# Optimization experiments

Hardware: AMD Instinct MI355X
Metric: run time of the kernel (lower is better)

## Reference

```python
import jax, jax.numpy as jnp
import numpy as np

HEADS = 8
DIM_HEAD = 64


def setup_inputs() -> dict:
    key = jax.random.key(0)
    ks = jax.random.split(key, 10)
    B, NQ, NK, D, INNER = 4, 2048, 2048, 1024, HEADS * DIM_HEAD
    w_scale = 0.02
    return {
        "x": jax.random.normal(ks[0], (B, NQ, D), jnp.float32),
        "context": jax.random.normal(ks[1], (B, NK, D), jnp.float32),
        "wq": jax.random.normal(ks[2], (D, INNER), jnp.float32) * w_scale,
        "bq": jax.random.normal(ks[3], (INNER,), jnp.float32) * w_scale,
        "wk": jax.random.normal(ks[4], (D, INNER), jnp.float32) * w_scale,
        "bk": jax.random.normal(ks[5], (INNER,), jnp.float32) * w_scale,
        "wv": jax.random.normal(ks[6], (D, INNER), jnp.float32) * w_scale,
        "bv": jax.random.normal(ks[7], (INNER,), jnp.float32) * w_scale,
        "wo": jax.random.normal(ks[8], (INNER, D), jnp.float32) * w_scale,
        "bo": jax.random.normal(ks[9], (D,), jnp.float32) * w_scale,
    }


def _split_heads(t):
    # [b, n, h*d] -> [b, h, n, d]
    b, n, _ = t.shape
    return t.reshape(b, n, HEADS, DIM_HEAD).transpose(0, 2, 1, 3)


def reference(x, context, wq, bq, wk, bk, wv, bv, wo, bo):
    scale = DIM_HEAD ** -0.5
    q = _split_heads(x @ wq + bq)        # [b, h, nq, d]
    k = _split_heads(context @ wk + bk)  # [b, h, nk, d]
    v = _split_heads(context @ wv + bv)  # [b, h, nk, d]
    sim = jnp.einsum('bhid,bhjd->bhij', q, k) * scale  # full score matrix, as in original
    attn = jax.nn.softmax(sim, axis=-1)
    out = jnp.einsum('bhij,bhjd->bhid', attn, v)       # [b, h, nq, d]
    b, h, n, d = out.shape
    out = out.transpose(0, 2, 1, 3).reshape(b, n, h * d)
    return out @ wo + bo
```

## Files before the change

kernel.cpp:

```cpp
#include <hip/hip_runtime.h>
#include <hip/hip_bf16.h>

typedef __attribute__((ext_vector_type(8))) short short8;
typedef __attribute__((ext_vector_type(4))) float f32x4;
typedef __attribute__((ext_vector_type(2))) unsigned uint2u;

__device__ __forceinline__ short f2bf(float f) {
  union { float f; unsigned u; } x; x.f = f;
  unsigned r = x.u + 0x7fffu + ((x.u >> 16) & 1u);
  return (short)(r >> 16);
}

__device__ __forceinline__ void gload16(const short* g, short* l) {
  __builtin_amdgcn_global_load_lds(
      (const __attribute__((address_space(1))) unsigned*)g,
      (__attribute__((address_space(3))) unsigned*)l, 16, 0, 0);
}

__global__ void cast2_bf16_kernel(const float* __restrict__ a,
                                  const float* __restrict__ b,
                                  short* __restrict__ dst) {
  int i = (blockIdx.x * 256 + threadIdx.x) * 4;
  const float* s = (i < (1 << 23)) ? a : b;
  int j = i & ((1 << 23) - 1);
  float4 f = *(const float4*)(s + j);
  union { short s[4]; uint2 u; } o;
  o.s[0] = f2bf(f.x); o.s[1] = f2bf(f.y);
  o.s[2] = f2bf(f.z); o.s[3] = f2bf(f.w);
  *(uint2*)(dst + i) = o.u;
}

__global__ __launch_bounds__(256) void transpose_cast4_kernel(
    const float* __restrict__ wq, const float* __restrict__ wk,
    const float* __restrict__ wv, const float* __restrict__ wo,
    short* __restrict__ wqt, short* __restrict__ wkt,
    short* __restrict__ wvt, short* __restrict__ wot) {
  __shared__ short tile[64][72];
  int z = blockIdx.z;
  const float* src = (z == 0) ? wq : (z == 1) ? wk : (z == 2) ? wv : wo;
  short* dst = (z == 0) ? wqt : (z == 1) ? wkt : (z == 2) ? wvt : wot;
  int R = (z < 3) ? 1024 : 512, C = (z < 3) ? 512 : 1024;
  int tpc = C >> 6;
  int bx = blockIdx.x % tpc, by = blockIdx.x / tpc;
  int r0 = by * 64, c0 = bx * 64;
  int tx = threadIdx.x & 15, ty = threadIdx.x >> 4;
#pragma unroll
  for (int i = 0; i < 4; i++) {
    int r = i * 16 + ty;
    float4 f = *(const float4*)(src + (size_t)(r0 + r) * C + c0 + tx * 4);
    union { short s[4]; uint2 u; } o;
    o.s[0] = f2bf(f.x); o.s[1] = f2bf(f.y);
    o.s[2] = f2bf(f.z); o.s[3] = f2bf(f.w);
    *(uint2*)&tile[r][tx * 4] = o.u;
  }
  __syncthreads();
#pragma unroll
  for (int i = 0; i < 4; i++) {
    int c = i * 16 + ty;
    union { short s[4]; uint2 u; } o;
#pragma unroll
    for (int k = 0; k < 4; k++) o.s[k] = tile[tx * 4 + k][c];
    *(uint2*)(dst + (size_t)(c0 + c) * R + r0 + tx * 4) = o.u;
  }
}

__device__ __forceinline__ void gemm_core(
    const short* __restrict__ A, const short* __restrict__ Bt, int K,
    int mblk, int nblk, short* sA, short* sB, f32x4 (&acc)[4][4]) {
  int tid = threadIdx.x;
  int lane = tid & 63, wave = tid >> 6;
  int quad = lane >> 4, l15 = lane & 15;
  int wm = (wave >> 1) * 64, wn = (wave & 1) * 64;
  int sub = lane >> 3, e8 = lane & 7;
  int swz = (e8 ^ sub) << 3;
  int s0 = (quad ^ (l15 & 7)) << 3;
  const short* Ag = A + (size_t)(mblk + 32 * wave + sub) * K + swz;
  const short* Bg = Bt + (size_t)(nblk + 32 * wave + sub) * K + swz;
  short* Al = sA + 4 * wave * 512;
  short* Bl = sB + 4 * wave * 512;

  for (int k0 = 0; k0 < K; k0 += 64) {
    __syncthreads();
#pragma unroll
    for (int t = 0; t < 4; t++) {
      gload16(Ag + (size_t)(8 * t) * K + k0, Al + t * 512);
      gload16(Bg + (size_t)(8 * t) * K + k0, Bl + t * 512);
    }
    __syncthreads();
#pragma unroll
    for (int h = 0; h < 2; h++) {
      int so = s0 ^ (h << 5);
      short8 af[4], bf[4];
#pragma unroll
      for (int mt = 0; mt < 4; mt++)
        af[mt] = *(const short8*)(&sA[(wm + mt * 16 + l15) * 64 + so]);
#pragma unroll
      for (int nt = 0; nt < 4; nt++)
        bf[nt] = *(const short8*)(&sB[(wn + nt * 16 + l15) * 64 + so]);
#pragma unroll
      for (int mt = 0; mt < 4; mt++)
#pragma unroll
        for (int nt = 0; nt < 4; nt++)
          acc[mt][nt] = __builtin_amdgcn_mfma_f32_16x16x32_bf16(
              af[mt], bf[nt], acc[mt][nt], 0, 0, 0);
    }
  }
}

__global__ __launch_bounds__(256) void gemm_qkv(
    const short* __restrict__ xb, const short* __restrict__ cb,
    const short* __restrict__ wqt, const short* __restrict__ wkt,
    const short* __restrict__ wvt,
    const float* __restrict__ bq, const float* __restrict__ bk,
    const float* __restrict__ bv,
    short* __restrict__ Qb, short* __restrict__ Kb, short* __restrict__ Vt) {
  __shared__ __align__(16) short sA[128 * 64];
  __shared__ __align__(16) short sB[128 * 64];
  int z = blockIdx.z;
  const short* A  = (z == 0) ? xb : cb;
  const short* Bt = (z == 0) ? wqt : (z == 1) ? wkt : wvt;
  const float* bias = (z == 0) ? bq : (z == 1) ? bk : bv;
  short* out = (z == 0) ? Qb : (z == 1) ? Kb : Vt;
  float scale = (z == 0) ? 0.18033688011112042f : 1.0f;
  int mblk = blockIdx.x * 128, nblk = blockIdx.y * 128;
  f32x4 acc[4][4] = {};
  gemm_core(A, Bt, 1024, mblk, nblk, sA, sB, acc);

  int lane = threadIdx.x & 63, wave = threadIdx.x >> 6;
  int quad = lane >> 4, l15 = lane & 15;
  int wm = (wave >> 1) * 64, wn = (wave & 1) * 64;
#pragma unroll
  for (int nt = 0; nt < 4; nt++) {
    int col = nblk + wn + nt * 16 + l15;
    float bias_v = bias[col];
    int h = col >> 6, dh = col & 63;
#pragma unroll
    for (int mt = 0; mt < 4; mt++)
#pragma unroll
      for (int r = 0; r < 4; r++) {
        int row = mblk + wm + mt * 16 + quad * 4 + r;
        float v = (acc[mt][nt][r] + bias_v) * scale;
        int b = row >> 11, n = row & 2047;
        size_t base = ((size_t)(b * 8 + h)) << 17;
        size_t idx = (z == 2) ? base + ((size_t)dh << 11) + n
                              : base + ((size_t)n << 6) + dh;
        out[idx] = f2bf(v);
      }
  }
}

__global__ __launch_bounds__(256) void gemm_out(
    const short* __restrict__ Ob, const short* __restrict__ wot,
    const float* __restrict__ bo, float* __restrict__ out) {
  __shared__ __align__(16) short sA[128 * 64];
  __shared__ __align__(16) short sB[128 * 64];
  int mblk = blockIdx.x * 128, nblk = blockIdx.y * 128;
  f32x4 acc[4][4] = {};
  gemm_core(Ob, wot, 512, mblk, nblk, sA, sB, acc);
  int lane = threadIdx.x & 63, wave = threadIdx.x >> 6;
  int quad = lane >> 4, l15 = lane & 15;
  int wm = (wave >> 1) * 64, wn = (wave & 1) * 64;
#pragma unroll
  for (int nt = 0; nt < 4; nt++) {
    int col = nblk + wn + nt * 16 + l15;
    float bias_v = bo[col];
#pragma unroll
    for (int mt = 0; mt < 4; mt++)
#pragma unroll
      for (int r = 0; r < 4; r++) {
        int row = mblk + wm + mt * 16 + quad * 4 + r;
        out[(size_t)row * 1024 + col] = acc[mt][nt][r] + bias_v;
      }
  }
}

__global__ __launch_bounds__(256, 2) void attn_kernel(
    const short* __restrict__ Qb, const short* __restrict__ Kb,
    const short* __restrict__ Vt, short* __restrict__ Ob) {
  __shared__ __align__(16) short sK[2 * 64 * 64];
  __shared__ __align__(16) short sV[2 * 64 * 64];
  int tid = threadIdx.x;
  int lane = tid & 63, wave = tid >> 6;
  int quad = lane >> 4, l15 = lane & 15;
  int bh = blockIdx.x & 31, qt = blockIdx.x >> 5;
  const short* Qp = Qb + ((size_t)bh << 17);
  const short* Kp = Kb + ((size_t)bh << 17);
  const short* Vp = Vt + ((size_t)bh << 17);
  int qrow0 = qt * 128 + wave * 32;

  short8 qf[2][2];
#pragma unroll
  for (int g = 0; g < 2; g++) {
    const short* qrow = Qp + (size_t)(qrow0 + g * 16 + l15) * 64;
    qf[g][0] = *(const short8*)(qrow + quad * 8);
    qf[g][1] = *(const short8*)(qrow + 32 + quad * 8);
  }

  int jk0 = 2 * wave, jk1 = 2 * wave + 1;
  int sub = lane >> 3;
  int e8  = lane & 7;
  int swz = (e8 ^ sub) << 3;
  const short* kg0 = Kp + (size_t)(8 * jk0 + sub) * 64 + e8 * 8;
  const short* kg1 = Kp + (size_t)(8 * jk1 + sub) * 64 + e8 * 8;
  const short* vg0 = Vp + (size_t)(8 * jk0 + sub) * 2048 + e8 * 8;
  const short* vg1 = Vp + (size_t)(8 * jk1 + sub) * 2048 + e8 * 8;
  int kw0 = (8 * jk0 + sub) * 64 + swz;
  int kw1 = (8 * jk1 + sub) * 64 + swz;

  int s0 = (quad ^ (l15 & 7)) << 3;
  int s1 = s0 ^ 32;

  f32x4 o[2][4] = {};
  float lsum[2] = {0.f, 0.f};

  uint4 rk0 = *(const uint4*)kg0, rk1 = *(const uint4*)kg1;
  uint4 rv0 = *(const uint4*)vg0, rv1 = *(const uint4*)vg1;
  *(uint4*)(sK + kw0) = rk0; *(uint4*)(sK + kw1) = rk1;
  *(uint4*)(sV + kw0) = rv0; *(uint4*)(sV + kw1) = rv1;
  rk0 = *(const uint4*)(kg0 + 4096); rk1 = *(const uint4*)(kg1 + 4096);
  rv0 = *(const uint4*)(vg0 + 64);   rv1 = *(const uint4*)(vg1 + 64);
  __syncthreads();

  for (int it = 0; it < 32; ++it) {
    const short* sKr = sK + (it & 1) * 4096;
    const short* sVr = sV + (it & 1) * 4096;
    if (it < 31) {
      short* sKw = sK + ((it & 1) ^ 1) * 4096;
      short* sVw = sV + ((it & 1) ^ 1) * 4096;
      *(uint4*)(sKw + kw0) = rk0; *(uint4*)(sKw + kw1) = rk1;
      *(uint4*)(sVw + kw0) = rv0; *(uint4*)(sVw + kw1) = rv1;
      if (it < 30) {
        size_t ko = (size_t)(it + 2) * 4096, vo = (size_t)(it + 2) * 64;
        rk0 = *(const uint4*)(kg0 + ko); rk1 = *(const uint4*)(kg1 + ko);
        rv0 = *(const uint4*)(vg0 + vo); rv1 = *(const uint4*)(vg1 + vo);
      }
    }
    unsigned xp[2][4][2];
#pragma unroll
    for (int jt = 0; jt < 4; jt++) {
      short8 k0 = *(const short8*)(&sKr[(jt * 16 + l15) * 64 + s0]);
      short8 k1 = *(const short8*)(&sKr[(jt * 16 + l15) * 64 + s1]);
#pragma unroll
      for (int g = 0; g < 2; g++) {
        f32x4 zz = {0.f, 0.f, 0.f, 0.f};
        zz = __builtin_amdgcn_mfma_f32_16x16x32_bf16(k0, qf[g][0], zz, 0, 0, 0);
        f32x4 st = __builtin_amdgcn_mfma_f32_16x16x32_bf16(k1, qf[g][1], zz, 0, 0, 0);
        float p0 = exp2f(st[0]), p1 = exp2f(st[1]);
        float p2 = exp2f(st[2]), p3 = exp2f(st[3]);
        lsum[g] += (p0 + p1) + (p2 + p3);
        union { __hip_bfloat162 b; unsigned u; } a0, a1;
        a0.b = __float22bfloat162_rn(make_float2(p0, p1));
        a1.b = __float22bfloat162_rn(make_float2(p2, p3));
        xp[g][jt][0] = a0.u; xp[g][jt][1] = a1.u;
      }
    }
    short8 pf[2][2];
#pragma unroll
    for (int g = 0; g < 2; g++) {
#pragma unroll
      for (int hb = 0; hb < 2; hb++) {
        unsigned x0 = xp[g][2 * hb][0], x1 = xp[g][2 * hb][1];
        unsigned x2 = xp[g][2 * hb + 1][0], x3 = xp[g][2 * hb + 1][1];
        uint2u r1 = __builtin_amdgcn_permlane32_swap(x0, x2, false, false);
        uint2u r2 = __builtin_amdgcn_permlane16_swap(r1[0], r1[1], false, false);
        uint2u r3 = __builtin_amdgcn_permlane32_swap(x1, x3, false, false);
        uint2u r4 = __builtin_amdgcn_permlane16_swap(r3[0], r3[1], false, false);
        union { unsigned u[4]; short8 s; } P;
        P.u[0] = r2[0]; P.u[1] = r4[0]; P.u[2] = r2[1]; P.u[3] = r4[1];
        pf[g][hb] = P.s;
      }
    }
#pragma unroll
    for (int nt = 0; nt < 4; nt++) {
      short8 v0 = *(const short8*)(&sVr[(nt * 16 + l15) * 64 + s0]);
      short8 v1 = *(const short8*)(&sVr[(nt * 16 + l15) * 64 + s1]);
#pragma unroll
      for (int g = 0; g < 2; g++) {
        o[g][nt] = __builtin_amdgcn_mfma_f32_16x16x32_bf16(v0, pf[g][0], o[g][nt], 0, 0, 0);
        o[g][nt] = __builtin_amdgcn_mfma_f32_16x16x32_bf16(v1, pf[g][1], o[g][nt], 0, 0, 0);
      }
    }
    if (it < 31) __syncthreads();
  }

  int b = bh >> 3, h = bh & 7;
#pragma unroll
  for (int g = 0; g < 2; g++) {
    float l = lsum[g];
    l += __shfl_xor(l, 16, 64);
    l += __shfl_xor(l, 32, 64);
    float inv = 1.0f / l;
    size_t rowbase = ((size_t)b * 2048 + qrow0 + g * 16 + l15) * 512 + h * 64 + quad * 4;
#pragma unroll
    for (int nt = 0; nt < 4; nt++) {
      union { short s[4]; uint2 u; } pk2;
#pragma unroll
      for (int r = 0; r < 4; r++) pk2.s[r] = f2bf(o[g][nt][r] * inv);
      *(uint2*)(Ob + rowbase + nt * 16) = pk2.u;
    }
  }
}

extern "C" void kernel_launch(void* const* d_in, const int* in_sizes, int n_in,
                              void* d_out, int out_size, void* d_ws, size_t ws_size,
                              hipStream_t stream) {
  const float* x   = (const float*)d_in[0];
  const float* ctx = (const float*)d_in[1];
  const float* wq  = (const float*)d_in[2];
  const float* bq  = (const float*)d_in[3];
  const float* wk  = (const float*)d_in[4];
  const float* bk  = (const float*)d_in[5];
  const float* wv  = (const float*)d_in[6];
  const float* bv  = (const float*)d_in[7];
  const float* wo  = (const float*)d_in[8];
  const float* bo  = (const float*)d_in[9];
  float* out = (float*)d_out;
  char* ws = (char*)d_ws;

  short* xb  = (short*)(ws);
  short* cb  = (short*)(ws + (16ull << 20));
  short* wqt = (short*)(ws + (32ull << 20));
  short* wkt = (short*)(ws + (33ull << 20));
  short* wvt = (short*)(ws + (34ull << 20));
  short* wot = (short*)(ws + (35ull << 20));
  short* Qb  = (short*)(ws + (36ull << 20));
  short* Kb  = (short*)(ws + (44ull << 20));
  short* Vt  = (short*)(ws + (52ull << 20));
  short* Ob  = (short*)(ws + (60ull << 20));

  cast2_bf16_kernel<<<16384, 256, 0, stream>>>(x, ctx, xb);
  transpose_cast4_kernel<<<dim3(128, 1, 4), 256, 0, stream>>>(
      wq, wk, wv, wo, wqt, wkt, wvt, wot);
  gemm_qkv<<<dim3(64, 4, 3), 256, 0, stream>>>(xb, cb, wqt, wkt, wvt,
                                               bq, bk, bv, Qb, Kb, Vt);
  attn_kernel<<<512, 256, 0, stream>>>(Qb, Kb, Vt, Ob);
  gemm_out<<<dim3(64, 8), 256, 0, stream>>>(Ob, wot, bo, out);
}
```

Baseline: 248.0 us.

## Vectorize GEMM epilogues via swapped MFMA operands, add setprio and hardware bf16 pack

```diff
diff --git a/kernel.cpp b/kernel.cpp
--- a/kernel.cpp
+++ b/kernel.cpp
@@ -11,10 +11,21 @@
   return (short)(r >> 16);
 }
 
+__device__ __forceinline__ unsigned cvt_pk_bf16(float a, float b) {
+  unsigned r;
+  asm("v_cvt_pk_bf16_f32 %0, %1, %2" : "=v"(r) : "v"(a), "v"(b));
+  return r;
+}
+
 __device__ __forceinline__ void gload16(const short* g, short* l) {
   __builtin_amdgcn_global_load_lds(
       (const __attribute__((address_space(1))) unsigned*)g,
       (__attribute__((address_space(3))) unsigned*)l, 16, 0, 0);
+}
+
+__device__ __forceinline__ void barrier_lgkm() {
+  asm volatile("s_waitcnt lgkmcnt(0)" ::: "memory");
+  __builtin_amdgcn_s_barrier();
 }
 
 __global__ void cast2_bf16_kernel(const float* __restrict__ a,
@@ -64,6 +75,7 @@
   }
 }
 
+template <bool SWAP>
 __device__ __forceinline__ void gemm_core(
     const short* __restrict__ A, const short* __restrict__ Bt, int K,
     int mblk, int nblk, short* sA, short* sB, f32x4 (&acc)[4][4]) {
@@ -100,9 +112,14 @@
 #pragma unroll
       for (int mt = 0; mt < 4; mt++)
 #pragma unroll
-        for (int nt = 0; nt < 4; nt++)
-          acc[mt][nt] = __builtin_amdgcn_mfma_f32_16x16x32_bf16(
-              af[mt], bf[nt], acc[mt][nt], 0, 0, 0);
+        for (int nt = 0; nt < 4; nt++) {
+          if (SWAP)
+            acc[mt][nt] = __builtin_amdgcn_mfma_f32_16x16x32_bf16(
+                bf[nt], af[mt], acc[mt][nt], 0, 0, 0);
+          else
+            acc[mt][nt] = __builtin_amdgcn_mfma_f32_16x16x32_bf16(
+                af[mt], bf[nt], acc[mt][nt], 0, 0, 0);
+        }
     }
   }
 }
@@ -123,29 +140,50 @@
   short* out = (z == 0) ? Qb : (z == 1) ? Kb : Vt;
   float scale = (z == 0) ? 0.18033688011112042f : 1.0f;
   int mblk = blockIdx.x * 128, nblk = blockIdx.y * 128;
-  f32x4 acc[4][4] = {};
-  gemm_core(A, Bt, 1024, mblk, nblk, sA, sB, acc);
-
   int lane = threadIdx.x & 63, wave = threadIdx.x >> 6;
   int quad = lane >> 4, l15 = lane & 15;
   int wm = (wave >> 1) * 64, wn = (wave & 1) * 64;
-#pragma unroll
-  for (int nt = 0; nt < 4; nt++) {
-    int col = nblk + wn + nt * 16 + l15;
-    float bias_v = bias[col];
-    int h = col >> 6, dh = col & 63;
-#pragma unroll
-    for (int mt = 0; mt < 4; mt++)
-#pragma unroll
-      for (int r = 0; r < 4; r++) {
-        int row = mblk + wm + mt * 16 + quad * 4 + r;
-        float v = (acc[mt][nt][r] + bias_v) * scale;
+
+  if (z == 2) {
+    f32x4 acc[4][4] = {};
+    gemm_core<false>(A, Bt, 1024, mblk, nblk, sA, sB, acc);
+#pragma unroll
+    for (int nt = 0; nt < 4; nt++) {
+      int col = nblk + wn + nt * 16 + l15;
+      float bias_v = bias[col];
+      int h = col >> 6, dh = col & 63;
+#pragma unroll
+      for (int mt = 0; mt < 4; mt++) {
+        int row0 = mblk + wm + mt * 16 + quad * 4;
+        int b = row0 >> 11, n0 = row0 & 2047;
+        size_t base = ((size_t)(b * 8 + h)) << 17;
+        union { short s[4]; uint2 u; } pk;
+#pragma unroll
+        for (int r = 0; r < 4; r++) pk.s[r] = f2bf(acc[mt][nt][r] + bias_v);
+        *(uint2*)(out + base + ((size_t)dh << 11) + n0) = pk.u;
+      }
+    }
+  } else {
+    f32x4 acc[4][4] = {};
+    gemm_core<true>(A, Bt, 1024, mblk, nblk, sA, sB, acc);
+#pragma unroll
+    for (int nt = 0; nt < 4; nt++) {
+      int colbase = nblk + wn + nt * 16 + quad * 4;
+      float4 b4 = *(const float4*)(bias + colbase);
+      int h = colbase >> 6, dh0 = colbase & 63;
+#pragma unroll
+      for (int mt = 0; mt < 4; mt++) {
+        int row = mblk + wm + mt * 16 + l15;
         int b = row >> 11, n = row & 2047;
         size_t base = ((size_t)(b * 8 + h)) << 17;
-        size_t idx = (z == 2) ? base + ((size_t)dh << 11) + n
-                              : base + ((size_t)n << 6) + dh;
-        out[idx] = f2bf(v);
-      }
+        union { short s[4]; uint2 u; } pk;
+        pk.s[0] = f2bf((acc[mt][nt][0] + b4.x) * scale);
+        pk.s[1] = f2bf((acc[mt][nt][1] + b4.y) * scale);
+        pk.s[2] = f2bf((acc[mt][nt][2] + b4.z) * scale);
+        pk.s[3] = f2bf((acc[mt][nt][3] + b4.w) * scale);
+        *(uint2*)(out + base + ((size_t)n << 6) + dh0) = pk.u;
+      }
+    }
   }
 }
 
@@ -156,21 +194,22 @@
   __shared__ __align__(16) short sB[128 * 64];
   int mblk = blockIdx.x * 128, nblk = blockIdx.y * 128;
   f32x4 acc[4][4] = {};
-  gemm_core(Ob, wot, 512, mblk, nblk, sA, sB, acc);
+  gemm_core<true>(Ob, wot, 512, mblk, nblk, sA, sB, acc);
   int lane = threadIdx.x & 63, wave = threadIdx.x >> 6;
   int quad = lane >> 4, l15 = lane & 15;
   int wm = (wave >> 1) * 64, wn = (wave & 1) * 64;
 #pragma unroll
   for (int nt = 0; nt < 4; nt++) {
-    int col = nblk + wn + nt * 16 + l15;
-    float bias_v = bo[col];
-#pragma unroll
-    for (int mt = 0; mt < 4; mt++)
-#pragma unroll
-      for (int r = 0; r < 4; r++) {
-        int row = mblk + wm + mt * 16 + quad * 4 + r;
-        out[(size_t)row * 1024 + col] = acc[mt][nt][r] + bias_v;
-      }
+    int colbase = nblk + wn + nt * 16 + quad * 4;
+    float4 b4 = *(const float4*)(bo + colbase);
+#pragma unroll
+    for (int mt = 0; mt < 4; mt++) {
+      int row = mblk + wm + mt * 16 + l15;
+      f32x4 v;
+      v[0] = acc[mt][nt][0] + b4.x; v[1] = acc[mt][nt][1] + b4.y;
+      v[2] = acc[mt][nt][2] + b4.z; v[3] = acc[mt][nt][3] + b4.w;
+      *(f32x4*)(out + (size_t)row * 1024 + colbase) = v;
+    }
   }
 }
 
@@ -182,7 +221,8 @@
   int tid = threadIdx.x;
   int lane = tid & 63, wave = tid >> 6;
   int quad = lane >> 4, l15 = lane & 15;
-  int bh = blockIdx.x & 31, qt = blockIdx.x >> 5;
+  int bh = blockIdx.x & 31;
+  int qt = blockIdx.x >> 5;
   const short* Qp = Qb + ((size_t)bh << 17);
   const short* Kp = Kb + ((size_t)bh << 17);
   const short* Vp = Vt + ((size_t)bh << 17);
@@ -219,7 +259,7 @@
   *(uint4*)(sV + kw0) = rv0; *(uint4*)(sV + kw1) = rv1;
   rk0 = *(const uint4*)(kg0 + 4096); rk1 = *(const uint4*)(kg1 + 4096);
   rv0 = *(const uint4*)(vg0 + 64);   rv1 = *(const uint4*)(vg1 + 64);
-  __syncthreads();
+  barrier_lgkm();
 
   for (int it = 0; it < 32; ++it) {
     const short* sKr = sK + (it & 1) * 4096;
@@ -230,7 +270,8 @@
       *(uint4*)(sKw + kw0) = rk0; *(uint4*)(sKw + kw1) = rk1;
       *(uint4*)(sVw + kw0) = rv0; *(uint4*)(sVw + kw1) = rv1;
       if (it < 30) {
-        size_t ko = (size_t)(it + 2) * 4096, vo = (size_t)(it + 2) * 64;
+        size_t ko = (size_t)(it + 2) * 4096;
+        size_t vo = (size_t)(it + 2) * 64;
         rk0 = *(const uint4*)(kg0 + ko); rk1 = *(const uint4*)(kg1 + ko);
         rv0 = *(const uint4*)(vg0 + vo); rv1 = *(const uint4*)(vg1 + vo);
       }
@@ -243,15 +284,15 @@
 #pragma unroll
       for (int g = 0; g < 2; g++) {
         f32x4 zz = {0.f, 0.f, 0.f, 0.f};
+        __builtin_amdgcn_s_setprio(1);
         zz = __builtin_amdgcn_mfma_f32_16x16x32_bf16(k0, qf[g][0], zz, 0, 0, 0);
         f32x4 st = __builtin_amdgcn_mfma_f32_16x16x32_bf16(k1, qf[g][1], zz, 0, 0, 0);
+        __builtin_amdgcn_s_setprio(0);
         float p0 = exp2f(st[0]), p1 = exp2f(st[1]);
         float p2 = exp2f(st[2]), p3 = exp2f(st[3]);
         lsum[g] += (p0 + p1) + (p2 + p3);
-        union { __hip_bfloat162 b; unsigned u; } a0, a1;
-        a0.b = __float22bfloat162_rn(make_float2(p0, p1));
-        a1.b = __float22bfloat162_rn(make_float2(p2, p3));
-        xp[g][jt][0] = a0.u; xp[g][jt][1] = a1.u;
+        xp[g][jt][0] = cvt_pk_bf16(p0, p1);
+        xp[g][jt][1] = cvt_pk_bf16(p2, p3);
       }
     }
     short8 pf[2][2];
@@ -270,6 +311,7 @@
         pf[g][hb] = P.s;
       }
     }
+    __builtin_amdgcn_s_setprio(1);
 #pragma unroll
     for (int nt = 0; nt < 4; nt++) {
       short8 v0 = *(const short8*)(&sVr[(nt * 16 + l15) * 64 + s0]);
@@ -280,7 +322,8 @@
         o[g][nt] = __builtin_amdgcn_mfma_f32_16x16x32_bf16(v1, pf[g][1], o[g][nt], 0, 0, 0);
       }
     }
-    if (it < 31) __syncthreads();
+    __builtin_amdgcn_s_setprio(0);
+    if (it < 31) barrier_lgkm();
   }
 
   int b = bh >> 3, h = bh & 7;
```

New measurement: 241.9 us. -2.5%, faster.
